# Performance work log

Measured on AMD Instinct MI355X. Metric: run time of the kernel, lower is better.

Reference implementation:

```python
import jax, jax.numpy as jnp
import numpy as np

B, T, C = 4, 2048, 768
H = 12
D = C // H  # 64
WIN = 256


def setup_inputs() -> dict:
    key = jax.random.key(0)
    ks = jax.random.split(key, 13)
    s = 0.02
    return {
        "x": jax.random.normal(ks[0], (B, T, C), dtype=jnp.float32),
        "window": WIN,
        "qkv_w": jax.random.normal(ks[1], (C, 3 * C), dtype=jnp.float32) * s,
        "qkv_b": jax.random.normal(ks[2], (3 * C,), dtype=jnp.float32) * s,
        "proj_w": jax.random.normal(ks[3], (C, C), dtype=jnp.float32) * s,
        "proj_b": jax.random.normal(ks[4], (C,), dtype=jnp.float32) * s,
        "Wr": jax.random.normal(ks[5], (D, D), dtype=jnp.float32) * s,
        "Ur": jax.random.normal(ks[6], (D, D), dtype=jnp.float32) * s,
        "Wz": jax.random.normal(ks[7], (D, D), dtype=jnp.float32) * s,
        "Wn": jax.random.normal(ks[8], (D, D), dtype=jnp.float32) * s,
        "Un": jax.random.normal(ks[9], (D, D), dtype=jnp.float32) * s,
        "gate_w": jax.random.normal(ks[10], (C, H), dtype=jnp.float32) * s,
        "gate_b": jnp.ones((H,), dtype=jnp.float32),
    }


def reference(x, window, qkv_w, qkv_b, proj_w, proj_b, Wr, Ur, Wz, Wn, Un, gate_w, gate_b):
    Bx, Tx, Cx = x.shape
    Hh = gate_w.shape[1]
    Dd = Cx // Hh

    qkv = x @ qkv_w + qkv_b                       # [B,T,3C]
    q, k, v = jnp.split(qkv, 3, axis=-1)
    def to_heads(t):
        return t.reshape(Bx, Tx, Hh, Dd).transpose(0, 2, 1, 3)  # [B,H,T,D]
    q, k, v = to_heads(q), to_heads(k), to_heads(v)

    # windowed attention (faithful to source masking: keys j with i <= j < i+window)
    scale = Dd ** -0.5
    scores = jnp.einsum('bhid,bhjd->bhij', q, k) * scale
    i = jnp.arange(Tx)[:, None]
    j = jnp.arange(Tx)[None, :]
    allowed = (j >= i) & ((j - i) < window)
    scores = jnp.where(allowed, scores, -jnp.inf)
    attn = jax.nn.softmax(scores, axis=-1)
    local_out = jnp.einsum('bhij,bhjd->bhid', attn, v)  # [B,H,T,D]

    # GRU-style recurrent scan over time
    kT = jnp.moveaxis(k, 2, 0)  # [T,B,H,D]
    vT = jnp.moveaxis(v, 2, 0)

    def step(h, kv):
        kt, vt = kv
        r = jax.nn.sigmoid(h @ Wr + kt @ Ur)
        z = jax.nn.sigmoid(h @ Wz + kt)
        n = jnp.tanh((r * h) @ Wn + kt @ Un)
        h_new = (1.0 - z) * h + z * (n * vt)
        return h_new, h_new

    h0 = jnp.zeros((Bx, Hh, Dd), dtype=x.dtype)
    _, hs = jax.lax.scan(step, h0, (kT, vT))     # [T,B,H,D]
    rnn_out = jnp.moveaxis(hs, 0, 2)              # [B,H,T,D]

    alpha = jax.nn.sigmoid(x @ gate_w + gate_b)   # [B,T,H]
    alpha = alpha.transpose(0, 2, 1)[..., None]   # [B,H,T,1]
    y = alpha * local_out + (1.0 - alpha) * rnn_out
    y = y.transpose(0, 2, 1, 3).reshape(Bx, Tx, Cx)
    return y @ proj_w + proj_b
```

## Files before the change

kernel.cpp:

```cpp
#include <hip/hip_runtime.h>

#define L2E 1.44269504088896f

typedef short bf16x8 __attribute__((ext_vector_type(8)));
typedef float f32x4 __attribute__((ext_vector_type(4)));

static __device__ __forceinline__ unsigned short f2bf(float f){
  unsigned u = __float_as_uint(f);
  unsigned r = (u + 0x7FFFu + ((u >> 16) & 1u)) >> 16;
  return (unsigned short)r;
}
static __device__ __forceinline__ unsigned pkbf(float a, float b){
#if __has_builtin(__builtin_amdgcn_cvt_pk_bf16_f32)
  auto v = __builtin_amdgcn_cvt_pk_bf16_f32(a, b);
  unsigned u; __builtin_memcpy(&u, &v, 4); return u;
#else
  return (unsigned)f2bf(a) | ((unsigned)f2bf(b) << 16);
#endif
}
static __device__ __forceinline__ bf16x8 pk8(float f0,float f1,float f2,float f3,
                                             float f4,float f5,float f6,float f7){
  unsigned t[4] = {pkbf(f0,f1), pkbf(f2,f3), pkbf(f4,f5), pkbf(f6,f7)};
  bf16x8 r; __builtin_memcpy(&r, t, 16); return r;
}
static __device__ __forceinline__ float b2f(unsigned short h){
  return __uint_as_float(((unsigned)h) << 16);
}
static __device__ __forceinline__ f32x4 mfma16(bf16x8 a, bf16x8 b, f32x4 c){
  return __builtin_amdgcn_mfma_f32_16x16x32_bf16(a, b, c, 0, 0, 0);
}
static __device__ __forceinline__ bf16x8 bz8(){
  bf16x8 z;
#pragma unroll
  for (int e = 0; e < 8; ++e) z[e] = 0;
  return z;
}
static __device__ __forceinline__ f32x4 fz4(){
  f32x4 z; z[0]=0.f; z[1]=0.f; z[2]=0.f; z[3]=0.f; return z;
}

typedef __attribute__((address_space(1))) const unsigned int guint;
typedef __attribute__((address_space(3))) unsigned int luint;
static __device__ __forceinline__ void gl16(const void* g, void* l){
  __builtin_amdgcn_global_load_lds((guint*)g, (luint*)l, 16, 0, 0);
}

__global__ __launch_bounds__(256) void k_pre(
    const float* __restrict__ x, unsigned short* __restrict__ xb,
    const float* __restrict__ qkv_w, unsigned short* __restrict__ wqkvT,
    const float* __restrict__ proj_w, unsigned short* __restrict__ wprojT,
    const float* __restrict__ Wr, const float* __restrict__ Wz, const float* __restrict__ Wn,
    const float* __restrict__ Ur, const float* __restrict__ Un, unsigned short* __restrict__ wpack)
{
  __shared__ float tile[64][65];
  int bid = blockIdx.x, tid = threadIdx.x;
  if (bid < 1024){
    int i = bid*256 + tid;
    for (; i < 1572864; i += 1024*256){
      float4 v = ((const float4*)x)[i];
      uint2 o; o.x = pkbf(v.x, v.y); o.y = pkbf(v.z, v.w);
      ((uint2*)xb)[i] = o;
    }
  } else if (bid < 1600){
    const float* W; unsigned short* WT; int K, N, bx, by;
    if (bid < 1456){ W = qkv_w; WT = wqkvT; K = 768; N = 2304; int t = bid - 1024; bx = t % 36; by = t / 36; }
    else           { W = proj_w; WT = wprojT; K = 768; N = 768;  int t = bid - 1456; bx = t % 12; by = t / 12; }
    int k0 = by*64, n0 = bx*64;
#pragma unroll
    for (int u = 0; u < 16; ++u){
      int id = tid + 256*u;
      int r = id >> 6, c = id & 63;
      tile[r][c] = W[(long)(k0 + r)*N + n0 + c];
    }
    __syncthreads();
#pragma unroll
    for (int u = 0; u < 16; ++u){
      int id = tid + 256*u;
      int cn = id >> 6, rk = id & 63;
      WT[(long)(n0 + cn)*K + k0 + rk] = f2bf(tile[rk][cn]);
    }
  } else {
    int idx = (bid - 1600)*256 + tid;
    if (idx < 2560){
      int lane = idx & 63, f = (idx >> 6) & 1, nt = (idx >> 7) & 3, mat = idx >> 9;
      const float* Ws[5] = {Wr, Wz, Wn, Ur, Un};
      const float  sc[5] = {-L2E, -L2E, 2.0f*L2E, 1.0f, 1.0f};
      const float* W = Ws[mat];
      float s = sc[mat];
      int q = lane >> 4, n = 16*nt + (lane & 15);
      unsigned short* dst = wpack + (((mat*4 + nt)*2 + f)*64 + lane)*8;
#pragma unroll
      for (int jj = 0; jj < 8; ++jj){
        int k = 32*f + 8*q + jj;
        dst[jj] = f2bf(W[k*64 + n] * s);
      }
    }
  }
}

__global__ __launch_bounds__(256) void k_gemm_qkv(
    const unsigned short* __restrict__ A, const unsigned short* __restrict__ BT,
    const float* __restrict__ bias,
    unsigned short* __restrict__ qh, unsigned short* __restrict__ kh, unsigned short* __restrict__ vh)
{
  __shared__ __align__(16) unsigned short smem[17408];
  unsigned short (*As)[64] = (unsigned short(*)[64])smem;
  unsigned short (*Bs)[64] = (unsigned short(*)[64])(smem + 8192);
  int id = blockIdx.y*18 + blockIdx.x;
  int xcd = id & 7, jj = id >> 3;
  int by = xcd*8 + (jj & 7);
  int bx = jj >> 3;
  int tid = threadIdx.x, lane = tid & 63, wv = tid >> 6;
  int wy = wv >> 1, wx = wv & 1;
  int m0 = by*128, n0 = bx*128;
  int qm = lane & 15, qq = lane >> 4;
  int px = qm & 7;
  int lsw = ((lane & 7) ^ ((lane >> 3) & 7))*8;
  const unsigned short* Ag = &A[(long)(m0 + 32*wv + (lane >> 3))*768 + lsw];
  const unsigned short* Bg = &BT[(long)(n0 + 32*wv + (lane >> 3))*768 + lsw];
  f32x4 acc[4][4];
#pragma unroll
  for (int i = 0; i < 4; ++i)
#pragma unroll
    for (int j = 0; j < 4; ++j) acc[i][j] = fz4();

  for (int kk = 0; kk < 768; kk += 64){
    __syncthreads();
#pragma unroll
    for (int u = 0; u < 4; ++u){
      gl16(Ag + (long)(8*u)*768 + kk, &As[32*wv + 8*u][0]);
      gl16(Bg + (long)(8*u)*768 + kk, &Bs[32*wv + 8*u][0]);
    }
    __syncthreads();
#pragma unroll
    for (int kf = 0; kf < 2; ++kf){
      bf16x8 af[4], bfr[4];
#pragma unroll
      for (int i = 0; i < 4; ++i){
        af[i]  = *(bf16x8*)&As[64*wy + 16*i + qm][((qq + 4*kf) ^ px)*8];
        bfr[i] = *(bf16x8*)&Bs[64*wx + 16*i + qm][((qq + 4*kf) ^ px)*8];
      }
#pragma unroll
      for (int i = 0; i < 4; ++i)
#pragma unroll
        for (int j = 0; j < 4; ++j) acc[i][j] = mfma16(af[i], bfr[j], acc[i][j]);
    }
  }
  int sec = bx / 6;
  unsigned short* dst = (sec == 0) ? qh : ((sec == 1) ? kh : vh);
  float scale = (sec == 0) ? 0.125f*L2E : 1.0f;
  int b = by >> 4, t0 = (by & 15)*128;
  __syncthreads();
#pragma unroll
  for (int j = 0; j < 4; ++j){
    int cc = 64*wx + 16*j + qm;
    float bv = bias[n0 + cc];
#pragma unroll
    for (int i = 0; i < 4; ++i){
      int tr = 64*wy + 16*i + 4*qq;
      unsigned a01 = pkbf((acc[i][j][0] + bv)*scale, (acc[i][j][1] + bv)*scale);
      unsigned a23 = pkbf((acc[i][j][2] + bv)*scale, (acc[i][j][3] + bv)*scale);
      smem[(tr + 0)*136 + cc] = (unsigned short)a01;
      smem[(tr + 1)*136 + cc] = (unsigned short)(a01 >> 16);
      smem[(tr + 2)*136 + cc] = (unsigned short)a23;
      smem[(tr + 3)*136 + cc] = (unsigned short)(a23 >> 16);
    }
  }
  __syncthreads();
  int hbase = (n0 - sec*768) >> 6;
#pragma unroll
  for (int rr = 0; rr < 8; ++rr){
    int tr = 32*wv + 4*rr + (lane >> 4);
    int cl = (lane & 15)*8;
    bf16x8 v = *(bf16x8*)&smem[tr*136 + cl];
    int hh = hbase + (cl >> 6), dd = cl & 63;
    *(bf16x8*)&dst[((long)(b*12 + hh)*2048 + t0 + tr)*64 + dd] = v;
  }
}

__global__ __launch_bounds__(256) void k_mid1(
    const unsigned short* __restrict__ kh, const unsigned short* __restrict__ vh,
    const unsigned short* __restrict__ wpack,
    uint2* __restrict__ kurp, uint2* __restrict__ kunp,
    uint2* __restrict__ ktp,  uint2* __restrict__ vp,
    unsigned short* __restrict__ vt,
    const float* __restrict__ x, const float* __restrict__ gw,
    const float* __restrict__ gb, float* __restrict__ alpha)
{
  __shared__ __align__(16) unsigned short mbuf[9312];
  int bid = blockIdx.x, tid = threadIdx.x, lane = tid & 63, wv = tid >> 6;
  if (bid < 384){
    int g = bid % 3, tt = bid / 3;
    int qm = lane & 15, qq = lane >> 4;
    bf16x8 UrF[4][2], UnF[4][2], If[2];
#pragma unroll
    for (int nt = 0; nt < 4; ++nt)
#pragma unroll
      for (int f = 0; f < 2; ++f){
        UrF[nt][f] = *(const bf16x8*)&wpack[(((3*4 + nt)*2 + f)*64 + lane)*8];
        UnF[nt][f] = *(const bf16x8*)&wpack[(((4*4 + nt)*2 + f)*64 + lane)*8];
      }
#pragma unroll
    for (int par = 0; par < 2; ++par){
      If[par] = bz8();
#pragma unroll
      for (int jj = 0; jj < 8; ++jj)
        If[par][jj] = (8*qq + jj == 16*par + qm) ? (short)0x3F80 : (short)0;
    }
    int bh = 16*g + qm;
#pragma unroll
    for (int i = 0; i < 4; ++i){
      int t = tt*16 + wv*4 + i;
      const unsigned short* kr = &kh[((long)bh*2048 + t)*64];
      const unsigned short* vr = &vh[((long)bh*2048 + t)*64];
      bf16x8 kf0 = *(const bf16x8*)&kr[8*qq];
      bf16x8 kf1 = *(const bf16x8*)&kr[32 + 8*qq];
      bf16x8 vf0 = *(const bf16x8*)&vr[8*qq];
      bf16x8 vf1 = *(const bf16x8*)&vr[32 + 8*qq];
      long obase = (long)((t*3 + g)*4)*64 + lane;
#pragma unroll
      for (int nt = 0; nt < 4; ++nt){
        f32x4 aur = mfma16(UrF[nt][0], kf0, fz4()); aur = mfma16(UrF[nt][1], kf1, aur);
        f32x4 aun = mfma16(UnF[nt][0], kf0, fz4()); aun = mfma16(UnF[nt][1], kf1, aun);
        f32x4 akt = mfma16(If[nt & 1], (nt < 2) ? kf0 : kf1, fz4());
        f32x4 avt = mfma16(If[nt & 1], (nt < 2) ? vf0 : vf1, fz4());
        uint2 o;
        o.x = pkbf(-L2E*aur[0], -L2E*aur[1]); o.y = pkbf(-L2E*aur[2], -L2E*aur[3]);
        kurp[obase + (long)nt*64] = o;
        o.x = pkbf(2.0f*L2E*aun[0], 2.0f*L2E*aun[1]); o.y = pkbf(2.0f*L2E*aun[2], 2.0f*L2E*aun[3]);
        kunp[obase + (long)nt*64] = o;
        o.x = pkbf(-L2E*akt[0], -L2E*akt[1]); o.y = pkbf(-L2E*akt[2], -L2E*akt[3]);
        ktp[obase + (long)nt*64] = o;
        o.x = pkbf(avt[0], avt[1]); o.y = pkbf(avt[2], avt[3]);
        vp[obase + (long)nt*64] = o;
      }
    }
  } else if (bid < 1920){
    int tvid = bid - 384;
    int bh = tvid >> 5, t0 = (tvid & 31)*64;
    unsigned short (*tl)[72] = (unsigned short(*)[72])mbuf;
#pragma unroll
    for (int u = 0; u < 2; ++u){
      int id = tid + 256*u;
      int r = id >> 3, gg = id & 7;
      *(bf16x8*)&tl[r][gg*8] = *(const bf16x8*)&vh[((long)bh*2048 + t0 + r)*64 + gg*8];
    }
    __syncthreads();
#pragma unroll
    for (int u = 0; u < 2; ++u){
      int id = tid + 256*u;
      int d = id >> 3, tg = id & 7;
      bf16x8 o;
#pragma unroll
      for (int e = 0; e < 8; ++e) o[e] = (short)tl[tg*8 + e][d];
      *(bf16x8*)&vt[((long)bh*64 + d)*2048 + t0 + tg*8] = o;
    }
  } else {
    int gid = bid - 1920;
    unsigned short (*gwt)[776] = (unsigned short(*)[776])mbuf;
    for (int i = tid; i < 9216; i += 256){
      int k = i / 12, h = i - 12*k;
      gwt[h][k] = f2bf(gw[i]);
    }
    __syncthreads();
    if (tid < 192){
      int r = gid*16 + tid/12;
      int h = tid % 12;
      const float4* xr = (const float4*)(x + (long)r*768);
      float acc = 0.f;
#pragma unroll 4
      for (int j = 0; j < 192; ++j){
        float4 a = xr[j];
        ushort4 w = *(const ushort4*)&gwt[h][4*j];
        acc += a.x*b2f(w.x) + a.y*b2f(w.y) + a.z*b2f(w.z) + a.w*b2f(w.w);
      }
      alpha[r*12 + h] = 1.0f / (1.0f + exp2f(-L2E*(acc + gb[h])));
    }
  }
}

__global__ __launch_bounds__(256, 4) void k_mid2(
    const uint2* __restrict__ kurp, const uint2* __restrict__ kunp,
    const uint2* __restrict__ ktp,  const uint2* __restrict__ vp,
    const unsigned short* __restrict__ wpack, unsigned short* __restrict__ rnn,
    const unsigned short* __restrict__ qh, const unsigned short* __restrict__ kh,
    const unsigned short* __restrict__ vt, const int* __restrict__ winp,
    unsigned short* __restrict__ lo)
{
  __shared__ __align__(16) unsigned short smem[20480];
  int tid = threadIdx.x, lane = tid & 63, wv = tid >> 6;
  int qm = lane & 15, qq = lane >> 4;
  int px = qm & 7;
  if (blockIdx.x < 384){
    unsigned short* rh_s = smem;
    unsigned short* h_s  = smem + 1024;
    int q = qq;
    int g = blockIdx.x % 3, chunk = blockIdx.x / 3;
    int tw = chunk*16;
    int t0 = (tw >= 24) ? (tw - 24) : 0;
    int t1 = tw + 16;
    bf16x8 WrA0 = *(const bf16x8*)&wpack[(((0*4 + wv)*2 + 0)*64 + lane)*8];
    bf16x8 WrA1 = *(const bf16x8*)&wpack[(((0*4 + wv)*2 + 1)*64 + lane)*8];
    bf16x8 WzA0 = *(const bf16x8*)&wpack[(((1*4 + wv)*2 + 0)*64 + lane)*8];
    bf16x8 WzA1 = *(const bf16x8*)&wpack[(((1*4 + wv)*2 + 1)*64 + lane)*8];
    bf16x8 WnA0 = *(const bf16x8*)&wpack[(((2*4 + wv)*2 + 0)*64 + lane)*8];
    bf16x8 WnA1 = *(const bf16x8*)&wpack[(((2*4 + wv)*2 + 1)*64 + lane)*8];
    int wcol  = qm*64 + (((2*wv + (q >> 1)) ^ px)*8) + 4*(q & 1);
    int rcol0 = qm*64 + ((q ^ px)*8);
    int rcol1 = qm*64 + (((q + 4) ^ px)*8);
    int sp = 4*wv + q;
    int bh2 = 16*g + sp, b2 = bh2/12, h2 = bh2 % 12;
    long rbase2 = ((long)b2*2048)*768 + h2*64 + 4*qm;
    int scol = sp*64 + (((qm >> 1) ^ (sp & 7))*8) + 4*(qm & 1);

    float hC[4] = {0.f, 0.f, 0.f, 0.f};
    bf16x8 hB0 = bz8(), hB1 = bz8();
    uint2 br0, bn0, bk0, bv0, br1, bn1, bk1, bv1;
    {
      long li = ((long)(t0*3 + g)*4 + wv)*64 + lane;
      br0 = kurp[li]; bn0 = kunp[li]; bk0 = ktp[li]; bv0 = vp[li];
      int tp = (t0 + 1 < t1) ? t0 + 1 : t0;
      long lj = ((long)(tp*3 + g)*4 + wv)*64 + lane;
      br1 = kurp[lj]; bn1 = kunp[lj]; bk1 = ktp[lj]; bv1 = vp[lj];
    }
    auto step = [&](int t, uint2& br, uint2& bn, uint2& bk, uint2& bv){
      f32x4 rp = mfma16(WrA0, hB0, fz4()); rp = mfma16(WrA1, hB1, rp);
      f32x4 zp = mfma16(WzA0, hB0, fz4()); zp = mfma16(WzA1, hB1, zp);
      unsigned short kra[4] = {(unsigned short)br.x, (unsigned short)(br.x>>16),
                               (unsigned short)br.y, (unsigned short)(br.y>>16)};
      unsigned short kna[4] = {(unsigned short)bn.x, (unsigned short)(bn.x>>16),
                               (unsigned short)bn.y, (unsigned short)(bn.y>>16)};
      unsigned short kta[4] = {(unsigned short)bk.x, (unsigned short)(bk.x>>16),
                               (unsigned short)bk.y, (unsigned short)(bk.y>>16)};
      unsigned short vva[4] = {(unsigned short)bv.x, (unsigned short)(bv.x>>16),
                               (unsigned short)bv.y, (unsigned short)(bv.y>>16)};
      int tn = t + 2; if (tn >= t1) tn = t1 - 1;
      long li = ((long)(tn*3 + g)*4 + wv)*64 + lane;
      br = kurp[li]; bn = kunp[li]; bk = ktp[li]; bv = vp[li];
      uint2 rhv;
      {
        float s0 = __builtin_amdgcn_rcpf(1.0f + exp2f(rp[0] + b2f(kra[0]))) * hC[0];
        float s1 = __builtin_amdgcn_rcpf(1.0f + exp2f(rp[1] + b2f(kra[1]))) * hC[1];
        float s2 = __builtin_amdgcn_rcpf(1.0f + exp2f(rp[2] + b2f(kra[2]))) * hC[2];
        float s3 = __builtin_amdgcn_rcpf(1.0f + exp2f(rp[3] + b2f(kra[3]))) * hC[3];
        rhv.x = pkbf(s0, s1); rhv.y = pkbf(s2, s3);
      }
      *(uint2*)&rh_s[wcol] = rhv;
      __syncthreads();
      bf16x8 rB0 = *(bf16x8*)&rh_s[rcol0];
      bf16x8 rB1 = *(bf16x8*)&rh_s[rcol1];
      f32x4 np = mfma16(WnA0, rB0, fz4()); np = mfma16(WnA1, rB1, np);
      float hN[4];
#pragma unroll
      for (int r = 0; r < 4; ++r){
        float z = __builtin_amdgcn_rcpf(1.0f + exp2f(zp[r] + b2f(kta[r])));
        float n = 1.0f - 2.0f*__builtin_amdgcn_rcpf(1.0f + exp2f(np[r] + b2f(kna[r])));
        hN[r] = (1.0f - z)*hC[r] + z*(n*b2f(vva[r]));
        hC[r] = hN[r];
      }
      uint2 hv; hv.x = pkbf(hN[0], hN[1]); hv.y = pkbf(hN[2], hN[3]);
      *(uint2*)&h_s[wcol] = hv;
      __syncthreads();
      hB0 = *(bf16x8*)&h_s[rcol0];
      hB1 = *(bf16x8*)&h_s[rcol1];
      if (t >= tw){
        ushort4 o = *(ushort4*)&h_s[scol];
        *(ushort4*)&rnn[rbase2 + (long)t*768] = o;
      }
    };
    for (int t = t0; t < t1; t += 2){
      step(t,     br0, bn0, bk0, bv0);
      step(t + 1, br1, bn1, bk1, bv1);
    }
  } else {
    int id = blockIdx.x - 384;
    int xcd = id & 7, jj = id >> 3;
    int bh = xcd*6 + (jj % 6);
    int q0 = (jj / 6)*64;
    int win = winp[0];
    int i0 = q0 + 16*wv;
    int irow = i0 + qm;
    const unsigned short* kbase = kh + (long)bh*2048*64;
    const unsigned short* vbase = vt + (long)bh*64*2048;
    {
      int lr = lane >> 3;
      int lsw = ((lane & 7) ^ lr)*8;
#pragma unroll
      for (int u = 0; u < 10; ++u){
        int row = 80*wv + 8*u;
        int gr = q0 + row + lr; if (gr > 2047) gr = 2047;
        gl16(&kbase[(long)gr*64 + lsw], &smem[row*64]);
      }
    }
    const unsigned short* qbase = qh + ((long)bh*2048 + i0)*64;
    bf16x8 qf0 = *(const bf16x8*)&qbase[qm*64 + 8*qq];
    bf16x8 qf1 = *(const bf16x8*)&qbase[qm*64 + 32 + 8*qq];
    __syncthreads();
    f32x4 S[17];
#pragma unroll
    for (int u = 0; u < 17; ++u){
      int row = 16*wv + 16*u + qm;
      bf16x8 kf0 = *(bf16x8*)&smem[row*64 + ((qq ^ px)*8)];
      bf16x8 kf1 = *(bf16x8*)&smem[row*64 + (((qq + 4) ^ px)*8)];
      f32x4 s = mfma16(kf0, qf0, fz4());
      S[u] = mfma16(kf1, qf1, s);
    }
    float ls = 0.f;
#pragma unroll
    for (int u = 0; u < 17; ++u){
      bool masked = (u == 0) || (16*u + 15 >= win) || (i0 + 16*u + 15 >= 2048);
      if (!masked){
#pragma unroll
        for (int r = 0; r < 4; ++r){
          float p = exp2f(S[u][r]);
          S[u][r] = p; ls += p;
        }
      } else {
        int j0 = i0 + 16*u + 4*qq;
#pragma unroll
        for (int r = 0; r < 4; ++r){
          int j = j0 + r;
          bool valid = (j >= irow) && ((j - irow) < win) && (j < 2048);
          float p = valid ? exp2f(S[u][r]) : 0.f;
          S[u][r] = p; ls += p;
        }
      }
    }
    ls += __shfl_xor(ls, 16, 64);
    ls += __shfl_xor(ls, 32, 64);
    float inv = __builtin_amdgcn_rcpf(ls);
    __syncthreads();
    unsigned short* ps = &smem[wv*4736];
    {
      uint2 z; z.x = 0; z.y = 0;
      *(uint2*)&ps[qm*296 + 272 + 4*qq] = z;
    }
#pragma unroll
    for (int u = 0; u < 17; ++u){
      uint2 o;
      o.x = pkbf(S[u][0]*inv, S[u][1]*inv);
      o.y = pkbf(S[u][2]*inv, S[u][3]*inv);
      *(uint2*)&ps[qm*296 + 16*u + 4*qq] = o;
    }
    f32x4 O[4];
#pragma unroll
    for (int n = 0; n < 4; ++n) O[n] = fz4();
#pragma unroll
    for (int fk = 0; fk < 9; ++fk){
      bf16x8 pa = *(bf16x8*)&ps[qm*296 + 32*fk + 8*qq];
      int kb = i0 + 32*fk + 8*qq; if (kb > 2040) kb = 2040;
#pragma unroll
      for (int nt = 0; nt < 4; ++nt){
        bf16x8 vb = *(const bf16x8*)&vbase[(long)(16*nt + qm)*2048 + kb];
        O[nt] = mfma16(pa, vb, O[nt]);
      }
    }
    unsigned short* lob = lo + (long)bh*2048*64;
#pragma unroll
    for (int nt = 0; nt < 4; ++nt){
      unsigned p01 = pkbf(O[nt][0], O[nt][1]);
      unsigned p23 = pkbf(O[nt][2], O[nt][3]);
      int d = 16*nt + qm;
      lob[(long)(i0 + 4*qq + 0)*64 + d] = (unsigned short)p01;
      lob[(long)(i0 + 4*qq + 1)*64 + d] = (unsigned short)(p01 >> 16);
      lob[(long)(i0 + 4*qq + 2)*64 + d] = (unsigned short)p23;
      lob[(long)(i0 + 4*qq + 3)*64 + d] = (unsigned short)(p23 >> 16);
    }
  }
}

__global__ __launch_bounds__(256) void k_gemm_proj(
    const unsigned short* __restrict__ lo, const unsigned short* __restrict__ rnn,
    const float* __restrict__ alpha,
    const unsigned short* __restrict__ BT, const float* __restrict__ bias,
    float* __restrict__ out)
{
  __shared__ __align__(16) unsigned short smem[16384];
  unsigned short (*As)[64] = (unsigned short(*)[64])smem;
  unsigned short (*Bs)[64] = (unsigned short(*)[64])(smem + 8192);
  int id = blockIdx.y*6 + blockIdx.x;
  int xcd = id & 7, jj = id >> 3;
  int by = xcd*8 + (jj % 8);
  int bx = jj / 8;
  int tid = threadIdx.x, lane = tid & 63, wv = tid >> 6;
  int wy = wv >> 1, wx = wv & 1;
  int m0 = by*128, n0 = bx*128;
  int qm = lane & 15, qq = lane >> 4;
  int px = qm & 7;
  int lsw = ((lane & 7) ^ ((lane >> 3) & 7))*8;
  const unsigned short* Bg = &BT[(long)(n0 + 32*wv + (lane >> 3))*768 + lsw];
  int r0 = m0 + 32*wv + (lane >> 3);
  f32x4 acc[4][4];
#pragma unroll
  for (int i = 0; i < 4; ++i)
#pragma unroll
    for (int j = 0; j < 4; ++j) acc[i][j] = fz4();
  for (int kk = 0; kk < 768; kk += 64){
    int h = kk >> 6;
    __syncthreads();
#pragma unroll
    for (int u = 0; u < 4; ++u)
      gl16(Bg + (long)(8*u)*768 + kk, &Bs[32*wv + 8*u][0]);
#pragma unroll
    for (int u = 0; u < 4; ++u){
      int r = r0 + 8*u;
      int bb = r >> 11, tt2 = r & 2047;
      bf16x8 lv = *(const bf16x8*)&lo[((long)(bb*12 + h)*2048 + tt2)*64 + lsw];
      bf16x8 rv = *(const bf16x8*)&rnn[(long)r*768 + kk + lsw];
      float a = alpha[r*12 + h];
      float f[8];
#pragma unroll
      for (int e = 0; e < 8; ++e){
        float lf = b2f((unsigned short)lv[e]);
        float rf = b2f((unsigned short)rv[e]);
        f[e] = rf + a*(lf - rf);
      }
      *(bf16x8*)&As[32*wv + 8*u + (lane >> 3)][(lane & 7)*8] =
          pk8(f[0], f[1], f[2], f[3], f[4], f[5], f[6], f[7]);
    }
    __syncthreads();
#pragma unroll
    for (int kf = 0; kf < 2; ++kf){
      bf16x8 af[4], bfr[4];
#pragma unroll
      for (int i = 0; i < 4; ++i){
        af[i]  = *(bf16x8*)&As[64*wy + 16*i + qm][((qq + 4*kf) ^ px)*8];
        bfr[i] = *(bf16x8*)&Bs[64*wx + 16*i + qm][((qq + 4*kf) ^ px)*8];
      }
#pragma unroll
      for (int i = 0; i < 4; ++i)
#pragma unroll
        for (int j = 0; j < 4; ++j) acc[i][j] = mfma16(af[i], bfr[j], acc[i][j]);
    }
  }
#pragma unroll
  for (int j = 0; j < 4; ++j){
    int c = n0 + 64*wx + 16*j + qm;
    float bv = bias[c];
#pragma unroll
    for (int i = 0; i < 4; ++i){
      int m = m0 + 64*wy + 16*i + 4*qq;
#pragma unroll
      for (int r = 0; r < 4; ++r)
        out[(long)(m + r)*768 + c] = acc[i][j][r] + bv;
    }
  }
}

extern "C" void kernel_launch(void* const* d_in, const int* in_sizes, int n_in,
                              void* d_out, int out_size, void* d_ws, size_t ws_size,
                              hipStream_t stream){
  const float* x      = (const float*)d_in[0];
  const int*   winp   = (const int*)d_in[1];
  const float* qkv_w  = (const float*)d_in[2];
  const float* qkv_b  = (const float*)d_in[3];
  const float* proj_w = (const float*)d_in[4];
  const float* proj_b = (const float*)d_in[5];
  const float* Wr     = (const float*)d_in[6];
  const float* Ur     = (const float*)d_in[7];
  const float* Wz     = (const float*)d_in[8];
  const float* Wn     = (const float*)d_in[9];
  const float* Un     = (const float*)d_in[10];
  const float* gw     = (const float*)d_in[11];
  const float* gb     = (const float*)d_in[12];
  float* out = (float*)d_out;

  char* ws = (char*)d_ws;
  size_t off = 0;
  auto alloc = [&](size_t b){ size_t r = off; off += (b + 255) & ~(size_t)255; return ws + r; };
  const size_t SZ = 12582912;
  unsigned short* xb     = (unsigned short*)alloc(SZ);
  unsigned short* wqkvT  = (unsigned short*)alloc(2304*768*2);
  unsigned short* wprojT = (unsigned short*)alloc(768*768*2);
  unsigned short* wpack  = (unsigned short*)alloc(40960);
  unsigned short* qh     = (unsigned short*)alloc(SZ);
  unsigned short* kh     = (unsigned short*)alloc(SZ);
  unsigned short* vh     = (unsigned short*)alloc(SZ);
  unsigned short* vtb    = (unsigned short*)alloc(SZ);
  uint2* kurp            = (uint2*)alloc(SZ);
  uint2* kunp            = (uint2*)alloc(SZ);
  uint2* ktp             = (uint2*)alloc(SZ);
  uint2* vpp             = (uint2*)alloc(SZ);
  unsigned short* lob    = (unsigned short*)alloc(SZ);
  unsigned short* rnnb   = (unsigned short*)alloc(SZ);
  float* alphab          = (float*)alloc(98304*4);

  k_pre<<<1610, 256, 0, stream>>>(x, xb, qkv_w, wqkvT, proj_w, wprojT, Wr, Wz, Wn, Ur, Un, wpack);
  k_gemm_qkv<<<dim3(18, 64), 256, 0, stream>>>(xb, wqkvT, qkv_b, qh, kh, vh);
  k_mid1<<<2432, 256, 0, stream>>>(kh, vh, wpack, kurp, kunp, ktp, vpp, vtb, x, gw, gb, alphab);
  k_mid2<<<1920, 256, 0, stream>>>(kurp, kunp, ktp, vpp, wpack, rnnb, qh, kh, vtb, winp, lob);
  k_gemm_proj<<<dim3(6, 64), 256, 0, stream>>>(lob, rnnb, alphab, wprojT, proj_b, out);
}
```

Before: 262.9 us.

## Move gate computation to pre kernel, use fast exp2, prefetch proj A operands

```diff
diff --git a/kernel.cpp b/kernel.cpp
--- a/kernel.cpp
+++ b/kernel.cpp
@@ -26,6 +26,13 @@
 static __device__ __forceinline__ float b2f(unsigned short h){
   return __uint_as_float(((unsigned)h) << 16);
 }
+static __device__ __forceinline__ float fexp2(float x){
+#if __has_builtin(__builtin_amdgcn_exp2f)
+  return __builtin_amdgcn_exp2f(x);
+#else
+  return exp2f(x);
+#endif
+}
 static __device__ __forceinline__ f32x4 mfma16(bf16x8 a, bf16x8 b, f32x4 c){
   return __builtin_amdgcn_mfma_f32_16x16x32_bf16(a, b, c, 0, 0, 0);
 }
@@ -50,9 +57,10 @@
     const float* __restrict__ qkv_w, unsigned short* __restrict__ wqkvT,
     const float* __restrict__ proj_w, unsigned short* __restrict__ wprojT,
     const float* __restrict__ Wr, const float* __restrict__ Wz, const float* __restrict__ Wn,
-    const float* __restrict__ Ur, const float* __restrict__ Un, unsigned short* __restrict__ wpack)
+    const float* __restrict__ Ur, const float* __restrict__ Un, unsigned short* __restrict__ wpack,
+    const float* __restrict__ gw, const float* __restrict__ gb, float* __restrict__ alpha)
 {
-  __shared__ float tile[64][65];
+  __shared__ __align__(16) char sraw[18624];
   int bid = blockIdx.x, tid = threadIdx.x;
   if (bid < 1024){
     int i = bid*256 + tid;
@@ -62,6 +70,7 @@
       ((uint2*)xb)[i] = o;
     }
   } else if (bid < 1600){
+    float (*tile)[65] = (float(*)[65])sraw;
     const float* W; unsigned short* WT; int K, N, bx, by;
     if (bid < 1456){ W = qkv_w; WT = wqkvT; K = 768; N = 2304; int t = bid - 1024; bx = t % 36; by = t / 36; }
     else           { W = proj_w; WT = wprojT; K = 768; N = 768;  int t = bid - 1456; bx = t % 12; by = t / 12; }
@@ -79,7 +88,7 @@
       int cn = id >> 6, rk = id & 63;
       WT[(long)(n0 + cn)*K + k0 + rk] = f2bf(tile[rk][cn]);
     }
-  } else {
+  } else if (bid < 1610){
     int idx = (bid - 1600)*256 + tid;
     if (idx < 2560){
       int lane = idx & 63, f = (idx >> 6) & 1, nt = (idx >> 7) & 3, mat = idx >> 9;
@@ -94,6 +103,27 @@
         int k = 32*f + 8*q + jj;
         dst[jj] = f2bf(W[k*64 + n] * s);
       }
+    }
+  } else {
+    int gid = bid - 1610;
+    unsigned short (*gwt)[776] = (unsigned short(*)[776])sraw;
+    for (int i = tid; i < 9216; i += 256){
+      int k = i / 12, h = i - 12*k;
+      gwt[h][k] = f2bf(gw[i]);
+    }
+    __syncthreads();
+    if (tid < 192){
+      int r = gid*16 + tid/12;
+      int h = tid % 12;
+      const float4* xr = (const float4*)(x + (long)r*768);
+      float acc = 0.f;
+#pragma unroll 4
+      for (int j = 0; j < 192; ++j){
+        float4 a = xr[j];
+        ushort4 w = *(const ushort4*)&gwt[h][4*j];
+        acc += a.x*b2f(w.x) + a.y*b2f(w.y) + a.z*b2f(w.z) + a.w*b2f(w.w);
+      }
+      alpha[r*12 + h] = 1.0f / (1.0f + fexp2(-L2E*(acc + gb[h])));
     }
   }
 }
@@ -183,11 +213,9 @@
     const unsigned short* __restrict__ wpack,
     uint2* __restrict__ kurp, uint2* __restrict__ kunp,
     uint2* __restrict__ ktp,  uint2* __restrict__ vp,
-    unsigned short* __restrict__ vt,
-    const float* __restrict__ x, const float* __restrict__ gw,
-    const float* __restrict__ gb, float* __restrict__ alpha)
+    unsigned short* __restrict__ vt)
 {
-  __shared__ __align__(16) unsigned short mbuf[9312];
+  __shared__ __align__(16) unsigned short mbuf[4608];
   int bid = blockIdx.x, tid = threadIdx.x, lane = tid & 63, wv = tid >> 6;
   if (bid < 384){
     int g = bid % 3, tt = bid / 3;
@@ -235,7 +263,7 @@
         vp[obase + (long)nt*64] = o;
       }
     }
-  } else if (bid < 1920){
+  } else {
     int tvid = bid - 384;
     int bh = tvid >> 5, t0 = (tvid & 31)*64;
     unsigned short (*tl)[72] = (unsigned short(*)[72])mbuf;
@@ -254,27 +282,6 @@
 #pragma unroll
       for (int e = 0; e < 8; ++e) o[e] = (short)tl[tg*8 + e][d];
       *(bf16x8*)&vt[((long)bh*64 + d)*2048 + t0 + tg*8] = o;
-    }
-  } else {
-    int gid = bid - 1920;
-    unsigned short (*gwt)[776] = (unsigned short(*)[776])mbuf;
-    for (int i = tid; i < 9216; i += 256){
-      int k = i / 12, h = i - 12*k;
-      gwt[h][k] = f2bf(gw[i]);
-    }
-    __syncthreads();
-    if (tid < 192){
-      int r = gid*16 + tid/12;
-      int h = tid % 12;
-      const float4* xr = (const float4*)(x + (long)r*768);
-      float acc = 0.f;
-#pragma unroll 4
-      for (int j = 0; j < 192; ++j){
-        float4 a = xr[j];
-        ushort4 w = *(const ushort4*)&gwt[h][4*j];
-        acc += a.x*b2f(w.x) + a.y*b2f(w.y) + a.z*b2f(w.z) + a.w*b2f(w.w);
-      }
-      alpha[r*12 + h] = 1.0f / (1.0f + exp2f(-L2E*(acc + gb[h])));
     }
   }
 }
@@ -339,10 +346,10 @@
       br = kurp[li]; bn = kunp[li]; bk = ktp[li]; bv = vp[li];
       uint2 rhv;
       {
-        float s0 = __builtin_amdgcn_rcpf(1.0f + exp2f(rp[0] + b2f(kra[0]))) * hC[0];
-        float s1 = __builtin_amdgcn_rcpf(1.0f + exp2f(rp[1] + b2f(kra[1]))) * hC[1];
-        float s2 = __builtin_amdgcn_rcpf(1.0f + exp2f(rp[2] + b2f(kra[2]))) * hC[2];
-        float s3 = __builtin_amdgcn_rcpf(1.0f + exp2f(rp[3] + b2f(kra[3]))) * hC[3];
+        float s0 = __builtin_amdgcn_rcpf(1.0f + fexp2(rp[0] + b2f(kra[0]))) * hC[0];
+        float s1 = __builtin_amdgcn_rcpf(1.0f + fexp2(rp[1] + b2f(kra[1]))) * hC[1];
+        float s2 = __builtin_amdgcn_rcpf(1.0f + fexp2(rp[2] + b2f(kra[2]))) * hC[2];
+        float s3 = __builtin_amdgcn_rcpf(1.0f + fexp2(rp[3] + b2f(kra[3]))) * hC[3];
         rhv.x = pkbf(s0, s1); rhv.y = pkbf(s2, s3);
       }
       *(uint2*)&rh_s[wcol] = rhv;
@@ -353,8 +360,8 @@
       float hN[4];
 #pragma unroll
       for (int r = 0; r < 4; ++r){
-        float z = __builtin_amdgcn_rcpf(1.0f + exp2f(zp[r] + b2f(kta[r])));
-        float n = 1.0f - 2.0f*__builtin_amdgcn_rcpf(1.0f + exp2f(np[r] + b2f(kna[r])));
+        float z = __builtin_amdgcn_rcpf(1.0f + fexp2(zp[r] + b2f(kta[r])));
+        float n = 1.0f - 2.0f*__builtin_amdgcn_rcpf(1.0f + fexp2(np[r] + b2f(kna[r])));
         hN[r] = (1.0f - z)*hC[r] + z*(n*b2f(vva[r]));
         hC[r] = hN[r];
       }
@@ -412,7 +419,7 @@
       if (!masked){
 #pragma unroll
         for (int r = 0; r < 4; ++r){
-          float p = exp2f(S[u][r]);
+          float p = fexp2(S[u][r]);
           S[u][r] = p; ls += p;
         }
       } else {
@@ -421,7 +428,7 @@
         for (int r = 0; r < 4; ++r){
           int j = j0 + r;
           bool valid = (j >= irow) && ((j - irow) < win) && (j < 2048);
-          float p = valid ? exp2f(S[u][r]) : 0.f;
+          float p = valid ? fexp2(S[u][r]) : 0.f;
           S[u][r] = p; ls += p;
         }
       }
@@ -490,35 +497,48 @@
   int lsw = ((lane & 7) ^ ((lane >> 3) & 7))*8;
   const unsigned short* Bg = &BT[(long)(n0 + 32*wv + (lane >> 3))*768 + lsw];
   int r0 = m0 + 32*wv + (lane >> 3);
+  int bb[4], tt2[4];
+#pragma unroll
+  for (int u = 0; u < 4; ++u){ int r = r0 + 8*u; bb[u] = r >> 11; tt2[u] = r & 2047; }
+
+  bf16x8 plv[4], prv[4]; float pa[4];
+  auto preload = [&](int kk){
+    int h = kk >> 6;
+#pragma unroll
+    for (int u = 0; u < 4; ++u){
+      int r = r0 + 8*u;
+      plv[u] = *(const bf16x8*)&lo[((long)(bb[u]*12 + h)*2048 + tt2[u])*64 + lsw];
+      prv[u] = *(const bf16x8*)&rnn[(long)r*768 + kk + lsw];
+      pa[u]  = alpha[r*12 + h];
+    }
+  };
+  preload(0);
+
   f32x4 acc[4][4];
 #pragma unroll
   for (int i = 0; i < 4; ++i)
 #pragma unroll
     for (int j = 0; j < 4; ++j) acc[i][j] = fz4();
+
   for (int kk = 0; kk < 768; kk += 64){
-    int h = kk >> 6;
-    __syncthreads();
+    __syncthreads();
+#pragma unroll
+    for (int u = 0; u < 4; ++u){
+      float f[8];
+#pragma unroll
+      for (int e = 0; e < 8; ++e){
+        float lf = b2f((unsigned short)plv[u][e]);
+        float rf = b2f((unsigned short)prv[u][e]);
+        f[e] = rf + pa[u]*(lf - rf);
+      }
+      *(bf16x8*)&As[32*wv + 8*u + (lane >> 3)][(lane & 7)*8] =
+          pk8(f[0], f[1], f[2], f[3], f[4], f[5], f[6], f[7]);
+    }
 #pragma unroll
     for (int u = 0; u < 4; ++u)
       gl16(Bg + (long)(8*u)*768 + kk, &Bs[32*wv + 8*u][0]);
-#pragma unroll
-    for (int u = 0; u < 4; ++u){
-      int r = r0 + 8*u;
-      int bb = r >> 11, tt2 = r & 2047;
-      bf16x8 lv = *(const bf16x8*)&lo[((long)(bb*12 + h)*2048 + tt2)*64 + lsw];
-      bf16x8 rv = *(const bf16x8*)&rnn[(long)r*768 + kk + lsw];
-      float a = alpha[r*12 + h];
-      float f[8];
-#pragma unroll
-      for (int e = 0; e < 8; ++e){
-        float lf = b2f((unsigned short)lv[e]);
-        float rf = b2f((unsigned short)rv[e]);
-        f[e] = rf + a*(lf - rf);
-      }
-      *(bf16x8*)&As[32*wv + 8*u + (lane >> 3)][(lane & 7)*8] =
-          pk8(f[0], f[1], f[2], f[3], f[4], f[5], f[6], f[7]);
-    }
-    __syncthreads();
+    __syncthreads();
+    if (kk + 64 < 768) preload(kk + 64);
 #pragma unroll
     for (int kf = 0; kf < 2; ++kf){
       bf16x8 af[4], bfr[4];
@@ -585,9 +605,9 @@
   unsigned short* rnnb   = (unsigned short*)alloc(SZ);
   float* alphab          = (float*)alloc(98304*4);
 
-  k_pre<<<1610, 256, 0, stream>>>(x, xb, qkv_w, wqkvT, proj_w, wprojT, Wr, Wz, Wn, Ur, Un, wpack);
+  k_pre<<<2122, 256, 0, stream>>>(x, xb, qkv_w, wqkvT, proj_w, wprojT, Wr, Wz, Wn, Ur, Un, wpack, gw, gb, alphab);
   k_gemm_qkv<<<dim3(18, 64), 256, 0, stream>>>(xb, wqkvT, qkv_b, qh, kh, vh);
-  k_mid1<<<2432, 256, 0, stream>>>(kh, vh, wpack, kurp, kunp, ktp, vpp, vtb, x, gw, gb, alphab);
+  k_mid1<<<1920, 256, 0, stream>>>(kh, vh, wpack, kurp, kunp, ktp, vpp, vtb);
   k_mid2<<<1920, 256, 0, stream>>>(kurp, kunp, ktp, vpp, wpack, rnnb, qh, kh, vtb, winp, lob);
   k_gemm_proj<<<dim3(6, 64), 256, 0, stream>>>(lob, rnnb, alphab, wprojT, proj_b, out);
 }
```

After: 257.1 us. 1.02x faster.
